# Kernel tuning notes

Hardware: AMD Instinct MI355X
Metric: run time of the kernel (lower is better)

The kernel has to match this reference:

```python
import jax, jax.numpy as jnp
import numpy as np

N_QUBITS = 6
N_LAYERS = 2
QSVT_DEGREE = 3
DT_RANK = max(N_QUBITS // 2, 1)
OUT_DIM = 3 * N_QUBITS
PI = np.float32(np.pi)
DT_MIN, DT_MAX = 1e-3, 0.1
BATCH, SEQ = 256, 512


def _ry_mat(theta):
    c = jnp.cos(theta / 2)
    s = jnp.sin(theta / 2)
    row0 = jnp.stack([c, -s], axis=-1)
    row1 = jnp.stack([s, c], axis=-1)
    return jnp.stack([row0, row1], axis=-2).astype(jnp.complex64)


def _rz_mat(theta):
    e = jnp.exp(-0.5j * theta.astype(jnp.complex64))
    z = jnp.zeros_like(e)
    row0 = jnp.stack([e, z], axis=-1)
    row1 = jnp.stack([z, jnp.conj(e)], axis=-1)
    return jnp.stack([row0, row1], axis=-2)


def _rx_mat(theta):
    c = jnp.cos(theta / 2).astype(jnp.complex64)
    s = jnp.sin(theta / 2).astype(jnp.complex64)
    row0 = jnp.stack([c, -1j * s], axis=-1)
    row1 = jnp.stack([-1j * s, c], axis=-1)
    return jnp.stack([row0, row1], axis=-2)


def _apply1(state, mat, w):
    # state: (B, 2, ..., 2) tensor over N_QUBITS axes; mat: (2,2) or batched (B,2,2)
    state = jnp.moveaxis(state, 1 + w, -1)
    if mat.ndim == 3:
        state = jnp.einsum('bij,b...j->b...i', mat, state)
    else:
        state = jnp.einsum('ij,b...j->b...i', mat, state)
    return jnp.moveaxis(state, -1, 1 + w)


def _cnot(state, c, t):
    state = jnp.moveaxis(state, (1 + c, 1 + t), (-2, -1))
    state = state.at[..., 1, :].set(state[..., 1, ::-1])
    return jnp.moveaxis(state, (-2, -1), (1 + c, 1 + t))


def _crx(state, theta, c, t):
    state = jnp.moveaxis(state, (1 + c, 1 + t), (-2, -1))
    m = _rx_mat(theta)
    state = state.at[..., 1, :].set(jnp.einsum('ij,...j->...i', m, state[..., 1, :]))
    return jnp.moveaxis(state, (-2, -1), (1 + c, 1 + t))


def _circuit(h, x, dt, circuit_params, poly_coeffs, qsvt_params):
    """Batched statevector simulation of the selective QSVT + unified ansatz qnode."""
    n = N_QUBITS
    B = h.shape[0]
    state = jnp.zeros((B,) + (2,) * n, jnp.complex64)
    state = state.at[(slice(None),) + (0,) * n].set(1.0 + 0.0j)
    # 1) state encoding RY(h[t-1])
    for i in range(n):
        state = _apply1(state, _ry_mat(h[:, i]), i)
    # 2) Delta-modulated QSVT: RZ rotations + bidirectional CNOT ring per degree
    qidx = 0
    n_qp = n * QSVT_DEGREE
    for deg in range(QSVT_DEGREE + 1):
        coeff = poly_coeffs[deg]
        for i in range(n):
            if qidx < n_qp:
                ang = coeff * dt[:, i] * qsvt_params[qidx] * PI
                qidx += 1
            else:
                ang = coeff * dt[:, i] * PI
            state = _apply1(state, _rz_mat(ang), i)
        for i in range(n - 1):
            state = _cnot(state, i, i + 1)
        state = _cnot(state, n - 1, 0)
        for i in range(n - 1, 0, -1):
            state = _cnot(state, i, i - 1)
    # 3) unified variational ansatz
    p = 0
    for _ in range(N_LAYERS):
        for i in range(n):
            state = _apply1(state, _rx_mat(circuit_params[p]), i)
            state = _apply1(state, _ry_mat(circuit_params[p + 1]), i)
            state = _apply1(state, _rz_mat(circuit_params[p + 2]), i)
            p += 3
        for i in range(n):
            state = _crx(state, circuit_params[p], i, (i + 1) % n)
            p += 1
        for i in range(n - 1, -1, -1):
            state = _crx(state, circuit_params[p], i, (i - 1) % n)
            p += 1
    # 4) Delta-modulated input RY(x * dt)
    for i in range(n):
        state = _apply1(state, _ry_mat(x[:, i] * dt[:, i]), i)
    # 5) Pauli X/Y/Z expectation values per qubit
    xs, ys, zs = [], [], []
    for i in range(n):
        s = jnp.moveaxis(state, 1 + i, 1).reshape(B, 2, -1)
        z = jnp.sum(jnp.conj(s[:, 0]) * s[:, 1], axis=-1)
        xs.append(2.0 * jnp.real(z))
        ys.append(2.0 * jnp.imag(z))
        zs.append(jnp.sum(jnp.abs(s[:, 0]) ** 2 - jnp.abs(s[:, 1]) ** 2, axis=-1))
    return jnp.stack(xs + ys + zs, axis=-1).astype(jnp.float32)  # (B, 3n)


def setup_inputs() -> dict:
    key = jax.random.key(0)
    ks = jax.random.split(key, 8)
    angles = jax.random.uniform(ks[0], (BATCH, SEQ, N_QUBITS), jnp.float32) * PI
    Wx = jax.random.normal(ks[1], (DT_RANK + 2 * N_QUBITS, N_QUBITS), jnp.float32) / np.float32(np.sqrt(N_QUBITS))
    Wdt = jax.random.normal(ks[2], (N_QUBITS, DT_RANK), jnp.float32) / np.float32(np.sqrt(DT_RANK))
    dt = jnp.exp(jax.random.uniform(ks[3], (N_QUBITS,), jnp.float32) * np.float32(np.log(DT_MAX) - np.log(DT_MIN)) + np.float32(np.log(DT_MIN)))
    bdt = dt + jnp.log(-jnp.expm1(-dt))
    poly_coeffs = jax.random.normal(ks[4], (QSVT_DEGREE + 1,), jnp.float32) * 0.1
    qsvt_params = jax.random.normal(ks[5], (N_QUBITS * QSVT_DEGREE,), jnp.float32) * 0.1
    circuit_params = jax.random.normal(ks[6], (5 * N_QUBITS * N_LAYERS,), jnp.float32) * 0.1
    D = jnp.ones((OUT_DIM,), jnp.float32)
    Wc = jax.random.normal(ks[7], (OUT_DIM, N_QUBITS), jnp.float32) / np.float32(np.sqrt(N_QUBITS))
    return {"angles": angles, "Wx": Wx, "Wdt": Wdt, "bdt": bdt, "poly_coeffs": poly_coeffs, "qsvt_params": qsvt_params, "circuit_params": circuit_params, "D": D, "Wc": Wc}


def reference(angles, Wx, Wdt, bdt, poly_coeffs, qsvt_params, circuit_params, D, Wc):
    x_dbc = angles @ Wx.T  # (B,S, dt_rank + 2n)
    dt_raw = x_dbc[..., :DT_RANK]
    # B slice computed in the original but never used in forward
    C = x_dbc[..., DT_RANK + N_QUBITS:]
    dt_angles = jnp.tanh(jax.nn.softplus(dt_raw @ Wdt.T + bdt)) * PI  # (B,S,n)
    # quantum part is detached in the original (detach().cpu() before the qnode)
    sg = jax.lax.stop_gradient
    xs = (jnp.moveaxis(sg(angles), 1, 0), jnp.moveaxis(sg(dt_angles), 1, 0))
    cp, pc, qp = sg(circuit_params), sg(poly_coeffs), sg(qsvt_params)
    h0 = jnp.zeros((angles.shape[0], N_QUBITS), jnp.float32)

    def step(h, xt):
        x_t, dt_t = xt
        meas = _circuit(h, x_t, dt_t, cp, pc, qp)
        return meas[:, 2 * N_QUBITS:], meas  # carry = PauliZ block

    _, meas = jax.lax.scan(step, h0, xs)
    h_full = jnp.moveaxis(meas, 0, 1)  # (B,S,3n)
    return (C @ Wc.T) * h_full + D * jnp.concatenate([angles] * 3, axis=-1)
```

## Files before the change

### kernel.cpp

```cpp
#include <hip/hip_runtime.h>
#include <math.h>

#define BATCH 256
#define SEQ 512
#define SDS 54
#define PI_F 3.14159265358979323846f

template<int CTRL>
__device__ __forceinline__ float fdpp(float v) {
    return __int_as_float(__builtin_amdgcn_mov_dpp(__float_as_int(v), CTRL, 0xF, 0xF, true));
}
template<int L>
__device__ __forceinline__ float rdl(float v) {
    return __int_as_float(__builtin_amdgcn_readlane(__float_as_int(v), L));
}
__device__ __forceinline__ float rdlv(float v, int l) {
    return __int_as_float(__builtin_amdgcn_readlane(__float_as_int(v), l));
}
template<int M>
__device__ __forceinline__ float shxm(float v) {
    if constexpr (M == 1)       return fdpp<0xB1>(v);
    else if constexpr (M == 2)  return fdpp<0x4E>(v);
    else if constexpr (M == 8)  return fdpp<0x128>(v);
    else if constexpr (M == 32) return __shfl_xor(v, 32, 64);
    else return __int_as_float(__builtin_amdgcn_ds_swizzle(__float_as_int(v), (M << 10) | 0x1F));
}
__device__ __forceinline__ float redsum64(float v) {
    v += fdpp<0x128>(v);
    v += fdpp<0x124>(v);
    v += fdpp<0x122>(v);
    v += fdpp<0x121>(v);
    return (rdl<0>(v) + rdl<16>(v)) + (rdl<32>(v) + rdl<48>(v));
}
__device__ __forceinline__ float xorf(float v, int m) {
    return __int_as_float(__float_as_int(v) ^ m);
}
__device__ __forceinline__ void wg_barrier_lds() {
    __builtin_amdgcn_sched_barrier(0);
    __builtin_amdgcn_s_waitcnt(0xC07F);
    __builtin_amdgcn_s_barrier();
    __builtin_amdgcn_sched_barrier(0);
}
__device__ __forceinline__ int permf(int x) {
    const int cs[11] = {0,1,2,3,4,5,5,4,3,2,1};
    const int ts[11] = {1,2,3,4,5,0,4,3,2,1,0};
#pragma unroll
    for (int k = 10; k >= 0; k--) {
        int cb = (x >> (5 - cs[k])) & 1;
        x ^= cb << (5 - ts[k]);
    }
    return x;
}
__device__ __forceinline__ void cmul4(const float* c,
    float vr, float vi, float ar, float ai, float br, float bi, float cr, float ci,
    float& nr, float& ni) {
    nr = c[0]*vr - c[1]*vi + c[2]*ar - c[3]*ai + c[4]*br - c[5]*bi + c[6]*cr - c[7]*ci;
    ni = c[0]*vi + c[1]*vr + c[2]*ai + c[3]*ar + c[4]*bi + c[5]*br + c[6]*ci + c[7]*cr;
}
__device__ __forceinline__ void ringapply(const float* rc,
    float vr, float vi, float br, float bi, float cr, float ci, float dr, float di,
    float& nr, float& ni) {
    nr = rc[0]*vr - rc[1]*bi - rc[2]*ci + rc[3]*dr;
    ni = rc[0]*vi + rc[1]*br + rc[2]*cr + rc[3]*di;
}

__global__ __launch_bounds__(256) void prep_kernel(
    const float* __restrict__ angles, const float* __restrict__ Wx,
    const float* __restrict__ Wdt, const float* __restrict__ bdt,
    const float* __restrict__ D, const float* __restrict__ Wc,
    float* __restrict__ sd)
{
    int gid = blockIdx.x * blockDim.x + threadIdx.x;
    if (gid >= BATCH * SEQ) return;
    const float* a = angles + (size_t)gid * 6;
    float ang[6];
#pragma unroll
    for (int i = 0; i < 6; i++) ang[i] = a[i];
    float dtr[3];
#pragma unroll
    for (int r = 0; r < 3; r++) {
        float s = 0.f;
#pragma unroll
        for (int k = 0; k < 6; k++) s += ang[k] * Wx[r * 6 + k];
        dtr[r] = s;
    }
    float* rec = sd + (size_t)gid * SDS;
    float dtv[6];
#pragma unroll
    for (int i = 0; i < 6; i++) {
        float x = bdt[i];
#pragma unroll
        for (int r = 0; r < 3; r++) x += dtr[r] * Wdt[i * 3 + r];
        float sp = (x > 15.f) ? x : log1pf(expf(x));
        dtv[i] = tanhf(sp) * PI_F;
        rec[i] = dtv[i];
        float th = ang[i] * dtv[i];
        rec[6 + i]  = cosf(th);
        rec[12 + i] = sinf(th);
    }
    float C[6];
#pragma unroll
    for (int i = 0; i < 6; i++) {
        float s = 0.f;
#pragma unroll
        for (int k = 0; k < 6; k++) s += ang[k] * Wx[(9 + i) * 6 + k];
        C[i] = s;
    }
#pragma unroll
    for (int j = 0; j < 18; j++) {
        float s = 0.f;
#pragma unroll
        for (int i = 0; i < 6; i++) s += C[i] * Wc[j * 6 + i];
        rec[18 + j] = s;
        rec[36 + j] = D[j] * ang[j % 6];
    }
}

__global__ __launch_bounds__(64) void umat_kernel(const float* __restrict__ cp,
                                                  float2* __restrict__ um)
{
    const int lane = threadIdx.x;
    const int col = blockIdx.x;
    int bitv[6];
#pragma unroll
    for (int i = 0; i < 6; i++) bitv[i] = (lane >> (5 - i)) & 1;

    float qc[2][3][8], rc[2][6][4];
#pragma unroll
    for (int l = 0; l < 2; l++) {
        float g00r[6], g00i[6], g01r[6], g01i[6], g10r[6], g10i[6], g11r[6], g11i[6];
#pragma unroll
        for (int i = 0; i < 6; i++) {
            float ax = cp[l * 30 + i * 3 + 0];
            float ay = cp[l * 30 + i * 3 + 1];
            float az = cp[l * 30 + i * 3 + 2];
            float ca = cosf(0.5f * ax), sa = sinf(0.5f * ax);
            float cb = cosf(0.5f * ay), sb = sinf(0.5f * ay);
            float cg = cosf(0.5f * az), sg = sinf(0.5f * az);
            float m00r = cb * ca, m00i =  sb * sa;
            float m01r = -sb * ca, m01i = -cb * sa;
            float m10r =  sb * ca, m10i = -cb * sa;
            float m11r =  cb * ca, m11i = -sb * sa;
            g00r[i] = cg * m00r + sg * m00i; g00i[i] = cg * m00i - sg * m00r;
            g01r[i] = cg * m01r + sg * m01i; g01i[i] = cg * m01i - sg * m01r;
            g10r[i] = cg * m10r - sg * m10i; g10i[i] = cg * m10i + sg * m10r;
            g11r[i] = cg * m11r - sg * m11i; g11i[i] = cg * m11i + sg * m11r;
        }
#pragma unroll
        for (int pp = 0; pp < 3; pp++) {
            int aq = 2 * pp, bq = 2 * pp + 1;
            float dar = bitv[aq] ? g11r[aq] : g00r[aq], dai = bitv[aq] ? g11i[aq] : g00i[aq];
            float oar = bitv[aq] ? g10r[aq] : g01r[aq], oai = bitv[aq] ? g10i[aq] : g01i[aq];
            float dbr = bitv[bq] ? g11r[bq] : g00r[bq], dbi = bitv[bq] ? g11i[bq] : g00i[bq];
            float obr = bitv[bq] ? g10r[bq] : g01r[bq], obi = bitv[bq] ? g10i[bq] : g01i[bq];
            qc[l][pp][0] = dar * dbr - dai * dbi;  qc[l][pp][1] = dar * dbi + dai * dbr;
            qc[l][pp][2] = oar * dbr - oai * dbi;  qc[l][pp][3] = oar * dbi + oai * dbr;
            qc[l][pp][4] = dar * obr - dai * obi;  qc[l][pp][5] = dar * obi + dai * obr;
            qc[l][pp][6] = oar * obr - oai * obi;  qc[l][pp][7] = oar * obi + oai * obr;
        }
        const int Aq[6] = {0, 2, 4, 5, 3, 1};
        const int Bq[6] = {1, 3, 5, 4, 2, 0};
#pragma unroll
        for (int o = 0; o < 6; o++) {
            float tha = (o < 3) ? cp[l * 30 + 18 + 2 * o]     : cp[l * 30 + 24 + 2 * (o - 3)];
            float thb = (o < 3) ? cp[l * 30 + 18 + 2 * o + 1] : cp[l * 30 + 24 + 2 * (o - 3) + 1];
            float ca = cosf(0.5f * tha), sa = sinf(0.5f * tha);
            float cb = cosf(0.5f * thb), sb = sinf(0.5f * thb);
            int ba = bitv[Aq[o]], bb = bitv[Bq[o]];
            float mx0 = ba ? ca : 1.f, sae = ba ? sa : 0.f;
            float ny0 = bb ? cb : 1.f, sbe = bb ? sb : 0.f;
            rc[l][o][0] = ny0 * mx0; rc[l][o][1] = -ny0 * sae;
            rc[l][o][2] = -mx0 * sbe; rc[l][o][3] = -sae * sbe;
        }
    }

    float re = (lane == col) ? 1.f : 0.f;
    float im = 0.f;
    auto p1q = [&](int mi, int mj, const float* c) {
        float ar = __shfl_xor(re, mi, 64), ai = __shfl_xor(im, mi, 64);
        float br = __shfl_xor(re, mj, 64), bi = __shfl_xor(im, mj, 64);
        float cr = __shfl_xor(re, mi | mj, 64), ci = __shfl_xor(im, mi | mj, 64);
        float nr, ni;
        cmul4(c, re, im, ar, ai, br, bi, cr, ci, nr, ni);
        re = nr; im = ni;
    };
    auto rng = [&](int mb, int mc, const float* c) {
        float br = __shfl_xor(re, mb, 64), bi = __shfl_xor(im, mb, 64);
        float cr = __shfl_xor(re, mc, 64), ci = __shfl_xor(im, mc, 64);
        float dr = __shfl_xor(re, mb | mc, 64), di = __shfl_xor(im, mb | mc, 64);
        float nr, ni;
        ringapply(c, re, im, br, bi, cr, ci, dr, di, nr, ni);
        re = nr; im = ni;
    };
#pragma unroll
    for (int l = 0; l < 2; l++) {
        p1q(32, 16, qc[l][0]);
        p1q(8, 4, qc[l][1]);
        p1q(2, 1, qc[l][2]);
        rng(16, 8, rc[l][0]);
        rng(4, 2, rc[l][1]);
        rng(1, 32, rc[l][2]);
        rng(2, 4, rc[l][3]);
        rng(8, 16, rc[l][4]);
        rng(32, 1, rc[l][5]);
    }
    um[(size_t)lane * 64 + col] = make_float2(re, im);
}

__global__ __launch_bounds__(512, 1) void step_kernel(
    const float* __restrict__ sd, const float* __restrict__ pc,
    const float* __restrict__ qp, const float2* __restrict__ um,
    float* __restrict__ out)
{
    __shared__ float2 sPart[8][64];
    __shared__ __align__(16) float sZX[12];
    const int tid = threadIdx.x;
    const int wave = tid >> 6;
    const int lane = tid & 63;
    const int b = blockIdx.x;

    int bitv[6];
#pragma unroll
    for (int i = 0; i < 6; i++) bitv[i] = (lane >> (5 - i)) & 1;
    int sflip[6];
#pragma unroll
    for (int q = 0; q < 6; q++) sflip[q] = bitv[q] ? (int)0x80000000 : 0;

    const int jbase = wave * 8;
    float2 row[8];
#pragma unroll
    for (int jj = 0; jj < 8; jj++) row[jj] = um[(size_t)lane * 64 + jbase + jj];

    float A[6], sel[6];
    {
        int x1 = permf(lane), x2 = permf(x1), x3 = permf(x2), x4 = permf(x3);
#pragma unroll
        for (int i = 0; i < 6; i++) {
            float u0 = pc[0] * PI_F * qp[0 * 6 + i];
            float u1 = pc[1] * PI_F * qp[1 * 6 + i];
            float u2 = pc[2] * PI_F * qp[2 * 6 + i];
            float u3 = pc[3] * PI_F;
            float t1 = ((x1 >> (5 - i)) & 1) ? 0.5f : -0.5f;
            float t2 = ((x2 >> (5 - i)) & 1) ? 0.5f : -0.5f;
            float t3 = ((x3 >> (5 - i)) & 1) ? 0.5f : -0.5f;
            float t4 = ((x4 >> (5 - i)) & 1) ? 0.5f : -0.5f;
            A[i] = u3 * t1 + u2 * t2 + u1 * t3 + u0 * t4;
            sel[i] = (float)((x4 >> (5 - i)) & 1);
        }
    }

    const float* sdb = sd + (size_t)b * SEQ * SDS;
    float* outb = out + (size_t)b * SEQ * 18;

    float h0 = 0.f, h1 = 0.f, h2 = 0.f, h3 = 0.f, h4 = 0.f, h5 = 0.f;

    float bufA[18], bufB[18];
    {
        const float2* p2 = (const float2*)sdb;
#pragma unroll
        for (int k = 0; k < 9; k++) {
            float2 v = p2[k];
            bufA[2 * k] = v.x; bufA[2 * k + 1] = v.y;
        }
    }

    auto body = [&](float (&cur)[18], float (&nxt)[18], int t) {
        {
            int tn = (t + 1 < SEQ) ? t + 1 : t;
            const float2* rn2 = (const float2*)(sdb + (size_t)tn * SDS);
#pragma unroll
            for (int k = 0; k < 9; k++) {
                float2 v = rn2[k];
                nxt[2 * k] = v.x; nxt[2 * k + 1] = v.y;
            }
        }

        float phi = A[0]*cur[0] + A[1]*cur[1] + A[2]*cur[2]
                  + A[3]*cur[3] + A[4]*cur[4] + A[5]*cur[5];
        float sph, cph;
        __sincosf(phi, &sph, &cph);

        float ss0, cc0, ss1, cc1, ss2, cc2, ss3, cc3, ss4, cc4, ss5, cc5;
        __sincosf(0.5f * h0, &ss0, &cc0);
        __sincosf(0.5f * h1, &ss1, &cc1);
        __sincosf(0.5f * h2, &ss2, &cc2);
        __sincosf(0.5f * h3, &ss3, &cc3);
        __sincosf(0.5f * h4, &ss4, &cc4);
        __sincosf(0.5f * h5, &ss5, &cc5);
        float f0 = fmaf(sel[0], ss0 - cc0, cc0);
        float f1 = fmaf(sel[1], ss1 - cc1, cc1);
        float f2 = fmaf(sel[2], ss2 - cc2, cc2);
        float f3 = fmaf(sel[3], ss3 - cc3, cc3);
        float f4 = fmaf(sel[4], ss4 - cc4, cc4);
        float f5 = fmaf(sel[5], ss5 - cc5, cc5);
        float prod = ((f0 * f1) * (f2 * f3)) * (f4 * f5);
        float pr = prod * cph, pi = prod * sph;

        float ar0 = 0.f, ai0 = 0.f, ar1 = 0.f, ai1 = 0.f;
#pragma unroll
        for (int jj = 0; jj < 8; jj += 2) {
            float sr0 = rdlv(pr, jbase + jj);
            float si0 = rdlv(pi, jbase + jj);
            float sr1 = rdlv(pr, jbase + jj + 1);
            float si1 = rdlv(pi, jbase + jj + 1);
            ar0 = fmaf(row[jj].x, sr0, ar0);
            ar0 = fmaf(-row[jj].y, si0, ar0);
            ai0 = fmaf(row[jj].x, si0, ai0);
            ai0 = fmaf(row[jj].y, sr0, ai0);
            ar1 = fmaf(row[jj + 1].x, sr1, ar1);
            ar1 = fmaf(-row[jj + 1].y, si1, ar1);
            ai1 = fmaf(row[jj + 1].x, si1, ai1);
            ai1 = fmaf(row[jj + 1].y, sr1, ai1);
        }
        sPart[wave][lane] = make_float2(ar0 + ar1, ai0 + ai1);
        wg_barrier_lds();
        float2 p0 = sPart[0][lane], p1 = sPart[1][lane];
        float2 p2 = sPart[2][lane], p3 = sPart[3][lane];
        float2 p4 = sPart[4][lane], p5 = sPart[5][lane];
        float2 p6 = sPart[6][lane], p7 = sPart[7][lane];
        float re = ((p0.x + p1.x) + (p2.x + p3.x)) + ((p4.x + p5.x) + (p6.x + p7.x));
        float im = ((p0.y + p1.y) + (p2.y + p3.y)) + ((p4.y + p5.y) + (p6.y + p7.y));

        float* o = outb + (size_t)t * 18;
        auto xy = [&](int q, int sf, float gr, float gi) {
            float X = redsum64(re * gr + im * gi);
            float Y = redsum64(xorf(re * gi - im * gr, sf));
            if (lane == 0) { sZX[6 + q] = X; o[6 + q] = X; o[12 + q] = Y; }
        };
        if (wave == 0) {
            float p = re * re + im * im;
            float Z0 = redsum64(xorf(p, sflip[0]));
            float Z1 = redsum64(xorf(p, sflip[1]));
            float Z2 = redsum64(xorf(p, sflip[2]));
            if (lane == 0) {
                sZX[0] = Z0; sZX[1] = Z1; sZX[2] = Z2;
                o[0] = Z0; o[1] = Z1; o[2] = Z2;
            }
        } else if (wave == 1) {
            float p = re * re + im * im;
            float Z3 = redsum64(xorf(p, sflip[3]));
            float Z4 = redsum64(xorf(p, sflip[4]));
            float Z5 = redsum64(xorf(p, sflip[5]));
            if (lane == 0) {
                sZX[3] = Z3; sZX[4] = Z4; sZX[5] = Z5;
                o[3] = Z3; o[4] = Z4; o[5] = Z5;
            }
        } else if (wave == 2) { xy(0, sflip[0], shxm<32>(re), shxm<32>(im)); }
          else if (wave == 3) { xy(1, sflip[1], shxm<16>(re), shxm<16>(im)); }
          else if (wave == 4) { xy(2, sflip[2], shxm<8>(re),  shxm<8>(im));  }
          else if (wave == 5) { xy(3, sflip[3], shxm<4>(re),  shxm<4>(im));  }
          else if (wave == 6) { xy(4, sflip[4], shxm<2>(re),  shxm<2>(im));  }
          else                { xy(5, sflip[5], shxm<1>(re),  shxm<1>(im));  }
        wg_barrier_lds();

        float4 v0 = ((const float4*)sZX)[0];
        float4 v1 = ((const float4*)sZX)[1];
        float4 v2 = ((const float4*)sZX)[2];
        h0 = cur[6]  * v0.x - cur[12] * v1.z;
        h1 = cur[7]  * v0.y - cur[13] * v1.w;
        h2 = cur[8]  * v0.z - cur[14] * v2.x;
        h3 = cur[9]  * v0.w - cur[15] * v2.y;
        h4 = cur[10] * v1.x - cur[16] * v2.z;
        h5 = cur[11] * v1.y - cur[17] * v2.w;
    };

    for (int t = 0; t < SEQ; t += 2) {
        body(bufA, bufB, t);
        body(bufB, bufA, t + 1);
    }
}

__global__ __launch_bounds__(256) void post_kernel(
    const float* __restrict__ sd, float* __restrict__ out)
{
    int gid = blockIdx.x * blockDim.x + threadIdx.x;
    if (gid >= BATCH * SEQ) return;
    const float* rec = sd + (size_t)gid * SDS;
    float* o = out + (size_t)gid * 18;

    float zxy[18];
    {
        const float2* o2 = (const float2*)o;
#pragma unroll
        for (int k = 0; k < 9; k++) {
            float2 v = o2[k];
            zxy[2 * k] = v.x; zxy[2 * k + 1] = v.y;
        }
    }
    float r[54];
    {
        const float2* r2 = (const float2*)rec;
#pragma unroll
        for (int k = 3; k < 27; k++) {
            float2 v = r2[k];
            r[2 * k] = v.x; r[2 * k + 1] = v.y;
        }
    }
    float res[18];
#pragma unroll
    for (int q = 0; q < 6; q++) {
        float Z = zxy[q], X = zxy[6 + q], Y = zxy[12 + q];
        float c = r[6 + q], s = r[12 + q];
        float px = c * X + s * Z;
        float hq = c * Z - s * X;
        res[q]      = fmaf(r[18 + q], px, r[36 + q]);
        res[6 + q]  = fmaf(r[24 + q], Y,  r[42 + q]);
        res[12 + q] = fmaf(r[30 + q], hq, r[48 + q]);
    }
    float2* ow = (float2*)o;
#pragma unroll
    for (int k = 0; k < 9; k++) ow[k] = make_float2(res[2 * k], res[2 * k + 1]);
}

extern "C" void kernel_launch(void* const* d_in, const int* in_sizes, int n_in,
                              void* d_out, int out_size, void* d_ws, size_t ws_size,
                              hipStream_t stream) {
    const float* angles = (const float*)d_in[0];
    const float* Wx     = (const float*)d_in[1];
    const float* Wdt    = (const float*)d_in[2];
    const float* bdt    = (const float*)d_in[3];
    const float* pc     = (const float*)d_in[4];
    const float* qp     = (const float*)d_in[5];
    const float* cp     = (const float*)d_in[6];
    const float* D      = (const float*)d_in[7];
    const float* Wc     = (const float*)d_in[8];
    float* sd  = (float*)d_ws;
    float2* um = (float2*)(sd + (size_t)BATCH * SEQ * SDS);
    float* out = (float*)d_out;

    umat_kernel<<<64, 64, 0, stream>>>(cp, um);
    prep_kernel<<<(BATCH * SEQ) / 256, 256, 0, stream>>>(angles, Wx, Wdt, bdt, D, Wc, sd);
    step_kernel<<<BATCH, 512, 0, stream>>>(sd, pc, qp, um, out);
    post_kernel<<<(BATCH * SEQ) / 256, 256, 0, stream>>>(sd, out);
}
```

Before: 720.9 us.

## Replace per-step reductions with butterfly transforms, halve block size, drop second barrier

Result: no change. 720.9 us (+0.0%).

```diff
diff --git a/kernel.cpp b/kernel.cpp
--- a/kernel.cpp
+++ b/kernel.cpp
@@ -95,8 +95,8 @@
         dtv[i] = tanhf(sp) * PI_F;
         rec[i] = dtv[i];
         float th = ang[i] * dtv[i];
-        rec[6 + i]  = cosf(th);
-        rec[12 + i] = sinf(th);
+        rec[6 + i]  = 0.5f * cosf(th);
+        rec[12 + i] = 0.5f * sinf(th);
     }
     float C[6];
 #pragma unroll
@@ -111,7 +111,7 @@
         float s = 0.f;
 #pragma unroll
         for (int i = 0; i < 6; i++) s += C[i] * Wc[j * 6 + i];
-        rec[18 + j] = s;
+        rec[18 + j] = (j < 6 || j >= 12) ? 2.f * s : s;
         rec[36 + j] = D[j] * ang[j % 6];
     }
 }
@@ -207,13 +207,12 @@
     um[(size_t)lane * 64 + col] = make_float2(re, im);
 }
 
-__global__ __launch_bounds__(512, 1) void step_kernel(
+__global__ __launch_bounds__(256, 1) void step_kernel(
     const float* __restrict__ sd, const float* __restrict__ pc,
     const float* __restrict__ qp, const float2* __restrict__ um,
     float* __restrict__ out)
 {
-    __shared__ float2 sPart[8][64];
-    __shared__ __align__(16) float sZX[12];
+    __shared__ float2 sPart[2][4][64];
     const int tid = threadIdx.x;
     const int wave = tid >> 6;
     const int lane = tid & 63;
@@ -223,13 +222,17 @@
 #pragma unroll
     for (int i = 0; i < 6; i++) bitv[i] = (lane >> (5 - i)) & 1;
     int sflip[6];
-#pragma unroll
-    for (int q = 0; q < 6; q++) sflip[q] = bitv[q] ? (int)0x80000000 : 0;
-
-    const int jbase = wave * 8;
-    float2 row[8];
-#pragma unroll
-    for (int jj = 0; jj < 8; jj++) row[jj] = um[(size_t)lane * 64 + jbase + jj];
+    float sgnf[6];
+#pragma unroll
+    for (int q = 0; q < 6; q++) {
+        sflip[q] = bitv[q] ? (int)0x80000000 : 0;
+        sgnf[q]  = bitv[q] ? -1.f : 1.f;
+    }
+
+    const int jbase = wave * 16;
+    float2 row[16];
+#pragma unroll
+    for (int jj = 0; jj < 16; jj++) row[jj] = um[(size_t)lane * 64 + jbase + jj];
 
     float A[6], sel[6];
     {
@@ -249,10 +252,27 @@
         }
     }
 
+    auto b6 = [&](float v) -> float {
+        float g;
+        g = shxm<1>(v);  v = fmaf(sgnf[5], v, g);
+        g = shxm<2>(v);  v = fmaf(sgnf[4], v, g);
+        g = shxm<4>(v);  v = fmaf(sgnf[3], v, g);
+        g = shxm<8>(v);  v = fmaf(sgnf[2], v, g);
+        g = shxm<16>(v); v = fmaf(sgnf[1], v, g);
+        g = shxm<32>(v); v = fmaf(sgnf[0], v, g);
+        return v;
+    };
+    auto b6c = [&](float& vr, float& vi) {
+#define BSTG(M, SI) { float gr = shxm<M>(vr), gi = shxm<M>(vi); \
+                      vr = fmaf(sgnf[SI], vr, gr); vi = fmaf(sgnf[SI], vi, gi); }
+        BSTG(1, 5) BSTG(2, 4) BSTG(4, 3) BSTG(8, 2) BSTG(16, 1) BSTG(32, 0)
+#undef BSTG
+    };
+
     const float* sdb = sd + (size_t)b * SEQ * SDS;
     float* outb = out + (size_t)b * SEQ * 18;
 
-    float h0 = 0.f, h1 = 0.f, h2 = 0.f, h3 = 0.f, h4 = 0.f, h5 = 0.f;
+    float hh0 = 0.f, hh1 = 0.f, hh2 = 0.f, hh3 = 0.f, hh4 = 0.f, hh5 = 0.f;
 
     float bufA[18], bufB[18];
     {
@@ -264,7 +284,7 @@
         }
     }
 
-    auto body = [&](float (&cur)[18], float (&nxt)[18], int t) {
+    auto body = [&](float (&cur)[18], float (&nxt)[18], int t, int pp) {
         {
             int tn = (t + 1 < SEQ) ? t + 1 : t;
             const float2* rn2 = (const float2*)(sdb + (size_t)tn * SDS);
@@ -281,12 +301,12 @@
         __sincosf(phi, &sph, &cph);
 
         float ss0, cc0, ss1, cc1, ss2, cc2, ss3, cc3, ss4, cc4, ss5, cc5;
-        __sincosf(0.5f * h0, &ss0, &cc0);
-        __sincosf(0.5f * h1, &ss1, &cc1);
-        __sincosf(0.5f * h2, &ss2, &cc2);
-        __sincosf(0.5f * h3, &ss3, &cc3);
-        __sincosf(0.5f * h4, &ss4, &cc4);
-        __sincosf(0.5f * h5, &ss5, &cc5);
+        __sincosf(hh0, &ss0, &cc0);
+        __sincosf(hh1, &ss1, &cc1);
+        __sincosf(hh2, &ss2, &cc2);
+        __sincosf(hh3, &ss3, &cc3);
+        __sincosf(hh4, &ss4, &cc4);
+        __sincosf(hh5, &ss5, &cc5);
         float f0 = fmaf(sel[0], ss0 - cc0, cc0);
         float f1 = fmaf(sel[1], ss1 - cc1, cc1);
         float f2 = fmaf(sel[2], ss2 - cc2, cc2);
@@ -298,7 +318,7 @@
 
         float ar0 = 0.f, ai0 = 0.f, ar1 = 0.f, ai1 = 0.f;
 #pragma unroll
-        for (int jj = 0; jj < 8; jj += 2) {
+        for (int jj = 0; jj < 16; jj += 2) {
             float sr0 = rdlv(pr, jbase + jj);
             float si0 = rdlv(pi, jbase + jj);
             float sr1 = rdlv(pr, jbase + jj + 1);
@@ -312,61 +332,70 @@
             ai1 = fmaf(row[jj + 1].x, si1, ai1);
             ai1 = fmaf(row[jj + 1].y, sr1, ai1);
         }
-        sPart[wave][lane] = make_float2(ar0 + ar1, ai0 + ai1);
+        sPart[pp][wave][lane] = make_float2(ar0 + ar1, ai0 + ai1);
         wg_barrier_lds();
-        float2 p0 = sPart[0][lane], p1 = sPart[1][lane];
-        float2 p2 = sPart[2][lane], p3 = sPart[3][lane];
-        float2 p4 = sPart[4][lane], p5 = sPart[5][lane];
-        float2 p6 = sPart[6][lane], p7 = sPart[7][lane];
-        float re = ((p0.x + p1.x) + (p2.x + p3.x)) + ((p4.x + p5.x) + (p6.x + p7.x));
-        float im = ((p0.y + p1.y) + (p2.y + p3.y)) + ((p4.y + p5.y) + (p6.y + p7.y));
+        float2 q0v = sPart[pp][0][lane], q1v = sPart[pp][1][lane];
+        float2 q2v = sPart[pp][2][lane], q3v = sPart[pp][3][lane];
+        float re = (q0v.x + q1v.x) + (q2v.x + q3v.x);
+        float im = (q0v.y + q1v.y) + (q2v.y + q3v.y);
+
+        float P  = fmaf(re, re, im * im);
+        float Wp = b6(P);
+        float Rr = re, Ri = im;
+        b6c(Rr, Ri);
+        float Q  = fmaf(Rr, Rr, Ri * Ri) * 0.015625f;
+        float Wq = b6(Q);
+
+        float Z0 = rdl<32>(Wp), Z1 = rdl<16>(Wp), Z2 = rdl<8>(Wp);
+        float Z3 = rdl<4>(Wp),  Z4 = rdl<2>(Wp),  Z5 = rdl<1>(Wp);
+        float X0 = rdl<32>(Wq), X1 = rdl<16>(Wq), X2 = rdl<8>(Wq);
+        float X3 = rdl<4>(Wq),  X4 = rdl<2>(Wq),  X5 = rdl<1>(Wq);
+
+        hh0 = cur[6]  * Z0 - cur[12] * X0;
+        hh1 = cur[7]  * Z1 - cur[13] * X1;
+        hh2 = cur[8]  * Z2 - cur[14] * X2;
+        hh3 = cur[9]  * Z3 - cur[15] * X3;
+        hh4 = cur[10] * Z4 - cur[16] * X4;
+        hh5 = cur[11] * Z5 - cur[17] * X5;
 
         float* o = outb + (size_t)t * 18;
-        auto xy = [&](int q, int sf, float gr, float gi) {
-            float X = redsum64(re * gr + im * gi);
-            float Y = redsum64(xorf(re * gi - im * gr, sf));
-            if (lane == 0) { sZX[6 + q] = X; o[6 + q] = X; o[12 + q] = Y; }
-        };
         if (wave == 0) {
-            float p = re * re + im * im;
-            float Z0 = redsum64(xorf(p, sflip[0]));
-            float Z1 = redsum64(xorf(p, sflip[1]));
-            float Z2 = redsum64(xorf(p, sflip[2]));
             if (lane == 0) {
-                sZX[0] = Z0; sZX[1] = Z1; sZX[2] = Z2;
-                o[0] = Z0; o[1] = Z1; o[2] = Z2;
+                float2* o2 = (float2*)o;
+                o2[0] = make_float2(Z0, Z1); o2[1] = make_float2(Z2, Z3);
+                o2[2] = make_float2(Z4, Z5); o2[3] = make_float2(X0, X1);
+                o2[4] = make_float2(X2, X3); o2[5] = make_float2(X4, X5);
             }
         } else if (wave == 1) {
-            float p = re * re + im * im;
-            float Z3 = redsum64(xorf(p, sflip[3]));
-            float Z4 = redsum64(xorf(p, sflip[4]));
-            float Z5 = redsum64(xorf(p, sflip[5]));
-            if (lane == 0) {
-                sZX[3] = Z3; sZX[4] = Z4; sZX[5] = Z5;
-                o[3] = Z3; o[4] = Z4; o[5] = Z5;
-            }
-        } else if (wave == 2) { xy(0, sflip[0], shxm<32>(re), shxm<32>(im)); }
-          else if (wave == 3) { xy(1, sflip[1], shxm<16>(re), shxm<16>(im)); }
-          else if (wave == 4) { xy(2, sflip[2], shxm<8>(re),  shxm<8>(im));  }
-          else if (wave == 5) { xy(3, sflip[3], shxm<4>(re),  shxm<4>(im));  }
-          else if (wave == 6) { xy(4, sflip[4], shxm<2>(re),  shxm<2>(im));  }
-          else                { xy(5, sflip[5], shxm<1>(re),  shxm<1>(im));  }
-        wg_barrier_lds();
-
-        float4 v0 = ((const float4*)sZX)[0];
-        float4 v1 = ((const float4*)sZX)[1];
-        float4 v2 = ((const float4*)sZX)[2];
-        h0 = cur[6]  * v0.x - cur[12] * v1.z;
-        h1 = cur[7]  * v0.y - cur[13] * v1.w;
-        h2 = cur[8]  * v0.z - cur[14] * v2.x;
-        h3 = cur[9]  * v0.w - cur[15] * v2.y;
-        h4 = cur[10] * v1.x - cur[16] * v2.z;
-        h5 = cur[11] * v1.y - cur[17] * v2.w;
+            float Gr = shxm<32>(Rr), Gi = shxm<32>(Ri);
+            float u0 = xorf(fmaf(-Ri, Gr, Rr * Gi), sflip[0]);
+            Gr = shxm<16>(Rr); Gi = shxm<16>(Ri);
+            float u1 = xorf(fmaf(-Ri, Gr, Rr * Gi), sflip[1]);
+            float Y0 = redsum64(u0) * -0.015625f;
+            float Y1 = redsum64(u1) * -0.015625f;
+            if (lane == 0) ((float2*)(o + 12))[0] = make_float2(Y0, Y1);
+        } else if (wave == 2) {
+            float Gr = shxm<8>(Rr), Gi = shxm<8>(Ri);
+            float u0 = xorf(fmaf(-Ri, Gr, Rr * Gi), sflip[2]);
+            Gr = shxm<4>(Rr); Gi = shxm<4>(Ri);
+            float u1 = xorf(fmaf(-Ri, Gr, Rr * Gi), sflip[3]);
+            float Y2 = redsum64(u0) * -0.015625f;
+            float Y3 = redsum64(u1) * -0.015625f;
+            if (lane == 0) ((float2*)(o + 14))[0] = make_float2(Y2, Y3);
+        } else {
+            float Gr = shxm<2>(Rr), Gi = shxm<2>(Ri);
+            float u0 = xorf(fmaf(-Ri, Gr, Rr * Gi), sflip[4]);
+            Gr = shxm<1>(Rr); Gi = shxm<1>(Ri);
+            float u1 = xorf(fmaf(-Ri, Gr, Rr * Gi), sflip[5]);
+            float Y4 = redsum64(u0) * -0.015625f;
+            float Y5 = redsum64(u1) * -0.015625f;
+            if (lane == 0) ((float2*)(o + 16))[0] = make_float2(Y4, Y5);
+        }
     };
 
     for (int t = 0; t < SEQ; t += 2) {
-        body(bufA, bufB, t);
-        body(bufB, bufA, t + 1);
+        body(bufA, bufB, t, 0);
+        body(bufB, bufA, t + 1, 1);
     }
 }
 
@@ -430,6 +459,6 @@
 
     umat_kernel<<<64, 64, 0, stream>>>(cp, um);
     prep_kernel<<<(BATCH * SEQ) / 256, 256, 0, stream>>>(angles, Wx, Wdt, bdt, D, Wc, sd);
-    step_kernel<<<BATCH, 512, 0, stream>>>(sd, pc, qp, um, out);
+    step_kernel<<<BATCH, 256, 0, stream>>>(sd, pc, qp, um, out);
     post_kernel<<<(BATCH * SEQ) / 256, 256, 0, stream>>>(sd, out);
 }
```
